# Kernel tuning notes

Hardware: AMD Instinct MI355X
Metric: run time of the kernel (lower is better)

Reference implementation:

```python
import jax, jax.numpy as jnp
import numpy as np

E, IN, OUT, T = 8, 4096, 4096, 8192
GS = IN  # groupsize=-1 -> groupsize = infeatures


def setup_inputs() -> dict:
    key = jax.random.key(0)
    k1, k2, k3, k4, k5 = jax.random.split(key, 5)
    x = jax.random.normal(k1, (T, IN), dtype=jnp.float16)
    indices = jax.random.randint(k2, (T,), 0, E, dtype=jnp.int32)
    # int32 words each packing 8 int4 nonzero values (2:4 sparse -> IN*OUT/2 values per expert)
    qweight = jax.random.randint(k3, (E, IN // 32, OUT * 16 // 8), 0, 2**31 - 1, dtype=jnp.int32)
    meta = jax.random.randint(k4, (E, OUT, IN // 16), 0, 2**15, dtype=jnp.int32).astype(jnp.int16)
    scales = (jax.random.uniform(k5, (E, IN // GS, OUT), dtype=jnp.float32) * 0.02 + 0.001).astype(jnp.float16)
    return {"x": x, "indices": indices, "qweight": qweight, "meta": meta, "scales": scales}


def _dequant_24(qweight, meta, scales):
    """Decode packed int4 + 2:4-sparsity metadata into dense fp32 weights (E, OUT, IN)."""
    # unpack 8 int4 nibbles per int32 word, symmetric zero-point 8
    nib = (qweight[..., None] >> (4 * jnp.arange(8, dtype=jnp.int32))) & 0xF  # (E, IN//32, 2*OUT, 8)
    vals = nib.reshape(E, IN // 2, OUT).transpose(0, 2, 1).astype(jnp.float32) - 8.0  # (E, OUT, IN//2)
    m = meta.astype(jnp.int32) & 0xFFFF
    sub = (m[..., None] >> (2 * jnp.arange(8, dtype=jnp.int32))) & 0x3  # (E, OUT, IN//16, 8)
    grp = (jnp.arange(8, dtype=jnp.int32) // 2) * 4                      # group-of-4 base within 16-block
    base = 16 * jnp.arange(IN // 16, dtype=jnp.int32)                    # 16-block base
    dense_col = (base[None, None, :, None] + grp[None, None, None, :] + sub).reshape(E, OUT, IN // 2)
    eidx = jnp.arange(E)[:, None, None]
    oidx = jnp.arange(OUT)[None, :, None]
    W = jnp.zeros((E, OUT, IN), jnp.float32).at[eidx, oidx, dense_col].add(vals)
    # per-group dequant scales: (E, IN//GS, OUT) -> (E, OUT, IN)
    s = jnp.repeat(scales.astype(jnp.float32), GS, axis=1).transpose(0, 2, 1)
    return W * s


def reference(x, indices, qweight, meta, scales):
    W = _dequant_24(qweight, meta, scales)  # (E, OUT, IN)
    y = jnp.zeros((x.shape[0], OUT), jnp.float32)
    for e in range(E):  # fixed small expert count
        xe = jnp.where((indices == e)[:, None], x, 0).astype(jnp.float32)
        y = y + xe @ W[e].T
    return y.astype(x.dtype)
```

## Files before the change

### kernel.cpp

```cpp
#include <hip/hip_runtime.h>

#define E_N   8
#define IN_N  4096
#define OUT_N 4096
#define T_N   8192

#define BM 256
#define BN 256
#define NT_K 64
#define NTHREADS 512

typedef unsigned short u16;
typedef __bf16 bf16_t;
typedef bf16_t bf16x8 __attribute__((ext_vector_type(8)));
typedef u16    u16x8  __attribute__((ext_vector_type(8)));
typedef float  f32x4  __attribute__((ext_vector_type(4)));

#define GLOAD16(gsrc, ldst) \
    __builtin_amdgcn_global_load_lds( \
        (const __attribute__((address_space(1))) unsigned int*)(gsrc), \
        (__attribute__((address_space(3))) unsigned int*)(ldst), 16, 0, 0)

__device__ int g_cnt[E_N];
__device__ int g_base[E_N];
__device__ int g_ids[T_N];
__device__ int g_meta_wide;
__device__ u16 g_W[(long)E_N * OUT_N * IN_N];
__device__ u16 g_xb[(long)T_N * IN_N];

__device__ __forceinline__ u16 f2bf(float f) {
    unsigned u = __builtin_bit_cast(unsigned, f);
    u += 0x7FFFu + ((u >> 16) & 1u);
    return (u16)(u >> 16);
}

__global__ void sort_tokens(const int* __restrict__ idx, const u16* __restrict__ meta16) {
    __shared__ int cnt[E_N], off[E_N];
    __shared__ int probe;
    const int tid = threadIdx.x;
    const int lane = tid & 63;
    if (tid == 0) probe = 0;
    if (tid < E_N) cnt[tid] = 0;
    __syncthreads();
    if (tid < 64) {
        unsigned v = meta16[2 * (tid * 131072) + 1];
        if (v) atomicOr(&probe, 1);
    }
    for (int t0 = tid - lane; t0 < T_N; t0 += blockDim.x) {
        const int t = t0 + lane;
        const int my = idx[t] & 7;
        #pragma unroll
        for (int e = 0; e < E_N; ++e) {
            unsigned long long m = __ballot(my == e);
            if (lane == 0 && m) atomicAdd(&cnt[e], __popcll(m));
        }
    }
    __syncthreads();
    if (tid == 0) {
        int s = 0;
        for (int e = 0; e < E_N; ++e) { g_cnt[e] = cnt[e]; g_base[e] = s; off[e] = s; s += cnt[e]; }
        g_meta_wide = (probe == 0) ? 1 : 0;
    }
    __syncthreads();
    for (int t0 = tid - lane; t0 < T_N; t0 += blockDim.x) {
        const int t = t0 + lane;
        const int my = idx[t] & 7;
        #pragma unroll
        for (int e = 0; e < E_N; ++e) {
            unsigned long long m = __ballot(my == e);
            if (my == e) {
                int below = __popcll(m & ((1ull << lane) - 1ull));
                int basep = 0;
                if (below == 0) basep = atomicAdd(&off[e], __popcll(m));
                int src = __ffsll((long long)m) - 1;
                basep = __shfl(basep, src);
                int p = basep + below;
                if (p >= 0 && p < T_N) g_ids[p] = t;
            }
        }
    }
}

__global__ __launch_bounds__(256, 4)
void xb_convert(const float* __restrict__ x) {
    const int p = blockIdx.x;
    int tok = g_ids[p];
    if ((unsigned)tok >= (unsigned)T_N) tok = 0;
    const float* src = x + (long)tok * IN_N;
    u16* dst = g_xb + (long)p * IN_N;
    const int tid = threadIdx.x;
    float va[16];
    #pragma unroll
    for (int c4 = 0; c4 < 4; ++c4) {
        float4 v = *reinterpret_cast<const float4*>(src + tid * 16 + c4 * 4);
        va[c4 * 4 + 0] = v.x; va[c4 * 4 + 1] = v.y; va[c4 * 4 + 2] = v.z; va[c4 * 4 + 3] = v.w;
    }
    unsigned wp[8];
    #pragma unroll
    for (int p8 = 0; p8 < 8; ++p8)
        wp[p8] = (unsigned)f2bf(va[2 * p8]) | ((unsigned)f2bf(va[2 * p8 + 1]) << 16);
    *reinterpret_cast<int4*>(dst + tid * 16)     = make_int4((int)wp[0], (int)wp[1], (int)wp[2], (int)wp[3]);
    *reinterpret_cast<int4*>(dst + tid * 16 + 8) = make_int4((int)wp[4], (int)wp[5], (int)wp[6], (int)wp[7]);
}

__global__ __launch_bounds__(256, 4)
void decode_w(const int* __restrict__ qw, const void* __restrict__ meta) {
    const int e   = blockIdx.z;
    const int kt0 = blockIdx.y * 4;
    const int o   = blockIdx.x * 256 + threadIdx.x;
    const bool mwide = (g_meta_wide != 0);
    unsigned mws[16];
    if (mwide) {
        const int* mp = (const int*)meta + ((long)e * OUT_N + o) * (IN_N / 16) + kt0 * 4;
        #pragma unroll
        for (int i = 0; i < 16; ++i) mws[i] = (unsigned)mp[i] & 0xFFFFu;
    } else {
        const u16* mp = (const u16*)meta + ((long)e * OUT_N + o) * (IN_N / 16) + kt0 * 4;
        #pragma unroll
        for (int i = 0; i < 16; ++i) mws[i] = mp[i];
    }
    const unsigned sh = (o & 7) << 2;
    const int osw = o & 7;
    #pragma unroll
    for (int ki = 0; ki < 4; ++ki) {
        const int kt = kt0 + ki;
        unsigned wp[32];
        #pragma unroll
        for (int gi = 0; gi < 4; ++gi) {
            const int g = kt * 4 + gi;
            const unsigned mw = mws[ki * 4 + gi];
            const int* qp = qw + ((e * (IN_N / 32) + (g >> 1)) << 13) + (o >> 3) + ((g & 1) << 12);
            int d[16];
            #pragma unroll
            for (int p = 0; p < 16; ++p) d[p] = 0;
            #pragma unroll
            for (int grp = 0; grp < 4; ++grp) {
                const unsigned w0 = (unsigned)qp[(2 * grp) * 512];
                const unsigned w1 = (unsigned)qp[(2 * grp + 1) * 512];
                const int v0 = (int)((w0 >> sh) & 0xF) - 8;
                const int v1 = (int)((w1 >> sh) & 0xF) - 8;
                const int s0 = (mw >> (4 * grp)) & 3;
                const int s1 = (mw >> (4 * grp + 2)) & 3;
                #pragma unroll
                for (int q = 0; q < 4; ++q) {
                    int t0 = (s0 == q) ? v0 : 0;
                    int t1 = (s1 == q) ? v1 : 0;
                    d[grp * 4 + q] = t0 + t1;
                }
            }
            #pragma unroll
            for (int p = 0; p < 8; ++p) {
                unsigned lo = __builtin_bit_cast(unsigned, (float)d[2 * p])     >> 16;
                unsigned hi = __builtin_bit_cast(unsigned, (float)d[2 * p + 1]) >> 16;
                wp[gi * 8 + p] = lo | (hi << 16);
            }
        }
        u16* wr = g_W + ((long)(e * 64 + kt) * OUT_N + o) * 64;
        #pragma unroll
        for (int h = 0; h < 8; ++h)
            *reinterpret_cast<int4*>(wr + (h ^ osw) * 8) =
                make_int4((int)wp[h * 4], (int)wp[h * 4 + 1], (int)wp[h * 4 + 2], (int)wp[h * 4 + 3]);
    }
}

__global__ __launch_bounds__(NTHREADS, 2)
void moe_gemm(const float* __restrict__ scales, float* __restrict__ y) {
    const int e = blockIdx.z;
    int cnt = g_cnt[e];
    if (cnt < 0) cnt = 0;
    if (cnt > T_N) cnt = T_N;
    const int m0 = blockIdx.y * BM;
    if (m0 >= cnt) return;
    const int n0 = blockIdx.x * BN;
    int base = g_base[e];
    if (base < 0) base = 0;
    if (base > T_N - cnt) base = T_N - cnt;

    __shared__ __align__(16) u16 As[2 * BM * 64];
    __shared__ __align__(16) u16 Bs[2 * BN * 64];

    const int tid  = threadIdx.x;
    const int lane = tid & 63;
    const int wid  = tid >> 6;
    const int wm   = wid >> 2;
    const int wn   = wid & 3;

    const int r_loc = tid >> 3;
    const int h_a   = (tid & 7) ^ (r_loc & 7);
    const u16* asrc[4];
    #pragma unroll
    for (int q = 0; q < 4; ++q) {
        long grow = (long)base + m0 + q * 64 + r_loc;
        if (grow > T_N - 1) grow = T_N - 1;
        asrc[q] = g_xb + grow * IN_N + h_a * 8;
    }
    const u16* bsrc = g_W + ((long)e * NT_K * OUT_N + n0) * 64 + (long)tid * 8;

#define STAGE_A(B_, KT_, HT_) do { \
    const int ktc_ = ((KT_) < NT_K) ? (KT_) : (NT_K - 1); \
    GLOAD16(asrc[(HT_)*2 + 0] + ktc_ * 64, &As[(B_)*16384 + ((HT_)*1024 + tid) * 8]); \
    GLOAD16(asrc[(HT_)*2 + 1] + ktc_ * 64, &As[(B_)*16384 + ((HT_)*1024 + 512 + tid) * 8]); \
} while (0)
#define STAGE_B(B_, KT_, HT_) do { \
    const int ktc_ = ((KT_) < NT_K) ? (KT_) : (NT_K - 1); \
    const u16* s_ = bsrc + (long)ktc_ * (OUT_N * 64) + (HT_) * 8192; \
    GLOAD16(s_,        &Bs[(B_)*16384 + ((HT_)*1024 + tid) * 8]); \
    GLOAD16(s_ + 4096, &Bs[(B_)*16384 + ((HT_)*1024 + 512 + tid) * 8]); \
} while (0)

    const int l15   = lane & 15;
    const int aoff0 = ((((lane >> 4))     ^ (lane & 7)) << 3);
    const int aoff1 = (((4 + (lane >> 4)) ^ (lane & 7)) << 3);
    const int arow0 = (wm * 128 + l15) * 64;
    const int brow0 = (wn * 64  + l15) * 64;

#define LD8(P_) __builtin_bit_cast(bf16x8, *reinterpret_cast<const u16x8*>(P_))
#define VM4 asm volatile("s_waitcnt vmcnt(4)" ::: "memory")
#define PH_NOP ((void)0)

    f32x4 acc[8][4];
    #pragma unroll
    for (int i = 0; i < 8; ++i)
        #pragma unroll
        for (int j = 0; j < 4; ++j) acc[i][j] = (f32x4){0.f, 0.f, 0.f, 0.f};

    bf16x8 aR[4][2];
    bf16x8 bR[2][2][2];

#define PH(B_, QM_, QN_, RDA_, RDB_, STAGE_STMT, TAIL_STMT) do { \
    if (RDA_) { _Pragma("unroll") for (int mf = 0; mf < 4; ++mf) { \
        const u16* p_ = &As[(B_)*16384 + arow0 + (QM_)*4096 + mf*1024]; \
        aR[mf][0] = LD8(p_ + aoff0); aR[mf][1] = LD8(p_ + aoff1); } } \
    if (RDB_) { _Pragma("unroll") for (int nf = 0; nf < 2; ++nf) { \
        const u16* p_ = &Bs[(B_)*16384 + brow0 + (QN_)*2048 + nf*1024]; \
        bR[QN_][nf][0] = LD8(p_ + aoff0); bR[QN_][nf][1] = LD8(p_ + aoff1); } } \
    STAGE_STMT; \
    __builtin_amdgcn_s_barrier(); \
    asm volatile("s_waitcnt lgkmcnt(0)" ::: "memory"); \
    __builtin_amdgcn_sched_barrier(0); \
    __builtin_amdgcn_s_setprio(1); \
    _Pragma("unroll") for (int ks = 0; ks < 2; ++ks) \
      _Pragma("unroll") for (int mf = 0; mf < 4; ++mf) \
        _Pragma("unroll") for (int nf = 0; nf < 2; ++nf) \
          acc[(QM_)*4 + mf][(QN_)*2 + nf] = __builtin_amdgcn_mfma_f32_16x16x32_bf16( \
              aR[mf][ks], bR[QN_][nf][ks], acc[(QM_)*4 + mf][(QN_)*2 + nf], 0, 0, 0); \
    __builtin_amdgcn_s_setprio(0); \
    TAIL_STMT; \
    __builtin_amdgcn_s_barrier(); \
} while (0)

    STAGE_A(0, 0, 0); STAGE_A(0, 0, 1);
    STAGE_B(0, 0, 0); STAGE_B(0, 0, 1);
    STAGE_B(1, 1, 0); STAGE_B(1, 1, 1);
    VM4;
    __builtin_amdgcn_s_barrier();

    for (int t = 0; t < NT_K / 2; ++t) {
        const int k1 = 2 * t + 1, k2 = 2 * t + 2, k3 = 2 * t + 3;
        PH(0, 0, 0, 1, 1, STAGE_A(1, k1, 0), PH_NOP);
        PH(0, 0, 1, 0, 1, STAGE_A(1, k1, 1), PH_NOP);
        PH(0, 1, 0, 1, 0, STAGE_B(0, k2, 0), PH_NOP);
        PH(0, 1, 1, 0, 0, STAGE_B(0, k2, 1), VM4);
        PH(1, 0, 0, 1, 1, STAGE_A(0, k2, 0), PH_NOP);
        PH(1, 0, 1, 0, 1, STAGE_A(0, k2, 1), PH_NOP);
        PH(1, 1, 0, 1, 0, STAGE_B(1, k3, 0), PH_NOP);
        PH(1, 1, 1, 0, 0, STAGE_B(1, k3, 1), VM4);
    }

    const int* toks = g_ids + base;
    float sc[4];
    #pragma unroll
    for (int nf = 0; nf < 4; ++nf)
        sc[nf] = scales[e * OUT_N + n0 + wn * 64 + nf * 16 + l15];
    #pragma unroll
    for (int mf = 0; mf < 8; ++mf) {
        #pragma unroll
        for (int r = 0; r < 4; ++r) {
            const int row = m0 + wm * 128 + mf * 16 + ((lane >> 4) << 2) + r;
            if (row >= cnt) continue;
            int tok = toks[row];
            if ((unsigned)tok >= (unsigned)T_N) continue;
            float* yrow = y + (long)tok * OUT_N;
            #pragma unroll
            for (int nf = 0; nf < 4; ++nf)
                yrow[n0 + wn * 64 + nf * 16 + l15] = acc[mf][nf][r] * sc[nf];
        }
    }
}

extern "C" void kernel_launch(void* const* d_in, const int* in_sizes, int n_in,
                              void* d_out, int out_size, void* d_ws, size_t ws_size,
                              hipStream_t stream) {
    const float* x      = nullptr;
    const int* indices  = nullptr;
    const int* qw       = nullptr;
    const void* meta    = nullptr;
    const float* scales = nullptr;
    int big_seen = 0;
    for (int i = 0; i < n_in; ++i) {
        long s = in_sizes[i];
        if (s == 33554432L)      x = (const float*)d_in[i];
        else if (s == 8192L)     indices = (const int*)d_in[i];
        else if (s == 32768L)    scales = (const float*)d_in[i];
        else if (s == 8388608L) {
            if (big_seen++ == 0)  qw = (const int*)d_in[i];
            else                  meta = d_in[i];
        }
    }
    if (!x || !indices || !qw || !meta || !scales) return;
    float* y = (float*)d_out;

    hipLaunchKernelGGL(sort_tokens, dim3(1), dim3(1024), 0, stream, indices, (const u16*)meta);
    hipLaunchKernelGGL(xb_convert, dim3(T_N), dim3(256), 0, stream, x);
    hipLaunchKernelGGL(decode_w, dim3(OUT_N / 256, 16, E_N), dim3(256), 0, stream, qw, meta);
    hipLaunchKernelGGL(moe_gemm, dim3(OUT_N / BN, T_N / BM, E_N), dim3(NTHREADS), 0, stream, scales, y);
}
```

Measured before the change: 648.1 us.

## Launch compact M-tile list with XCD swizzle and restage A/B loads

sort_tokens now builds a compact list of (expert, m0) tiles, and the GEMM launches a flat 640-block grid instead of the mostly-empty E×T/BM×N grid. Block IDs are swizzled so that neighbouring tiles land on the same XCD (block mod 8), which should improve L2 reuse. The load pipeline also changes: full A and B tiles for the next k-step are issued together in two of the eight phases, waiting at vmcnt(8), instead of being spread across all phases. This removes the launch cost of empty blocks but puts loads in bursts and assumes at most 64 M-tiles, which only holds for 8 experts and 8192 tokens.

```diff
diff --git a/kernel.cpp b/kernel.cpp
--- a/kernel.cpp
+++ b/kernel.cpp
@@ -9,6 +9,7 @@
 #define BN 256
 #define NT_K 64
 #define NTHREADS 512
+#define MAXMT 64
 
 typedef unsigned short u16;
 typedef __bf16 bf16_t;
@@ -25,6 +26,9 @@
 __device__ int g_base[E_N];
 __device__ int g_ids[T_N];
 __device__ int g_meta_wide;
+__device__ int g_mt_e[MAXMT];
+__device__ int g_mt_m0[MAXMT];
+__device__ int g_nmt;
 __device__ u16 g_W[(long)E_N * OUT_N * IN_N];
 __device__ u16 g_xb[(long)T_N * IN_N];
 
@@ -60,6 +64,10 @@
         int s = 0;
         for (int e = 0; e < E_N; ++e) { g_cnt[e] = cnt[e]; g_base[e] = s; off[e] = s; s += cnt[e]; }
         g_meta_wide = (probe == 0) ? 1 : 0;
+        int n = 0;
+        for (int e = 0; e < E_N; ++e)
+            for (int m0 = 0; m0 < cnt[e] && n < MAXMT; m0 += BM) { g_mt_e[n] = e; g_mt_m0[n] = m0; ++n; }
+        g_nmt = n;
     }
     __syncthreads();
     for (int t0 = tid - lane; t0 < T_N; t0 += blockDim.x) {
@@ -165,13 +173,17 @@
 
 __global__ __launch_bounds__(NTHREADS, 2)
 void moe_gemm(const float* __restrict__ scales, float* __restrict__ y) {
-    const int e = blockIdx.z;
+    const int blk = blockIdx.x;
+    const int swz = (blk & 7) * 80 + (blk >> 3);
+    const int mIdx = swz >> 4, nIdx = swz & 15;
+    if (mIdx >= g_nmt) return;
+    const int e  = g_mt_e[mIdx];
+    const int m0 = g_mt_m0[mIdx];
+    const int n0 = nIdx * BN;
     int cnt = g_cnt[e];
     if (cnt < 0) cnt = 0;
     if (cnt > T_N) cnt = T_N;
-    const int m0 = blockIdx.y * BM;
     if (m0 >= cnt) return;
-    const int n0 = blockIdx.x * BN;
     int base = g_base[e];
     if (base < 0) base = 0;
     if (base > T_N - cnt) base = T_N - cnt;
@@ -196,16 +208,18 @@
     }
     const u16* bsrc = g_W + ((long)e * NT_K * OUT_N + n0) * 64 + (long)tid * 8;
 
-#define STAGE_A(B_, KT_, HT_) do { \
-    const int ktc_ = ((KT_) < NT_K) ? (KT_) : (NT_K - 1); \
-    GLOAD16(asrc[(HT_)*2 + 0] + ktc_ * 64, &As[(B_)*16384 + ((HT_)*1024 + tid) * 8]); \
-    GLOAD16(asrc[(HT_)*2 + 1] + ktc_ * 64, &As[(B_)*16384 + ((HT_)*1024 + 512 + tid) * 8]); \
+#define STAGE_A4(B_, KT_) do { \
+    GLOAD16(asrc[0] + (KT_) * 64, &As[(B_)*16384 + tid * 8]); \
+    GLOAD16(asrc[1] + (KT_) * 64, &As[(B_)*16384 + (512 + tid) * 8]); \
+    GLOAD16(asrc[2] + (KT_) * 64, &As[(B_)*16384 + (1024 + tid) * 8]); \
+    GLOAD16(asrc[3] + (KT_) * 64, &As[(B_)*16384 + (1536 + tid) * 8]); \
 } while (0)
-#define STAGE_B(B_, KT_, HT_) do { \
-    const int ktc_ = ((KT_) < NT_K) ? (KT_) : (NT_K - 1); \
-    const u16* s_ = bsrc + (long)ktc_ * (OUT_N * 64) + (HT_) * 8192; \
-    GLOAD16(s_,        &Bs[(B_)*16384 + ((HT_)*1024 + tid) * 8]); \
-    GLOAD16(s_ + 4096, &Bs[(B_)*16384 + ((HT_)*1024 + 512 + tid) * 8]); \
+#define STAGE_B4(B_, KT_) do { \
+    const u16* s_ = bsrc + (long)(KT_) * (OUT_N * 64); \
+    GLOAD16(s_,         &Bs[(B_)*16384 + tid * 8]); \
+    GLOAD16(s_ + 4096,  &Bs[(B_)*16384 + (512 + tid) * 8]); \
+    GLOAD16(s_ + 8192,  &Bs[(B_)*16384 + (1024 + tid) * 8]); \
+    GLOAD16(s_ + 12288, &Bs[(B_)*16384 + (1536 + tid) * 8]); \
 } while (0)
 
     const int l15   = lane & 15;
@@ -215,7 +229,7 @@
     const int brow0 = (wn * 64  + l15) * 64;
 
 #define LD8(P_) __builtin_bit_cast(bf16x8, *reinterpret_cast<const u16x8*>(P_))
-#define VM4 asm volatile("s_waitcnt vmcnt(4)" ::: "memory")
+#define VM8 asm volatile("s_waitcnt vmcnt(8)" ::: "memory")
 #define PH_NOP ((void)0)
 
     f32x4 acc[8][4];
@@ -249,22 +263,22 @@
     __builtin_amdgcn_s_barrier(); \
 } while (0)
 
-    STAGE_A(0, 0, 0); STAGE_A(0, 0, 1);
-    STAGE_B(0, 0, 0); STAGE_B(0, 0, 1);
-    STAGE_B(1, 1, 0); STAGE_B(1, 1, 1);
-    VM4;
+    STAGE_A4(0, 0); STAGE_B4(0, 0);
+    STAGE_A4(1, 1); STAGE_B4(1, 1);
+    VM8;
     __builtin_amdgcn_s_barrier();
 
     for (int t = 0; t < NT_K / 2; ++t) {
-        const int k1 = 2 * t + 1, k2 = 2 * t + 2, k3 = 2 * t + 3;
-        PH(0, 0, 0, 1, 1, STAGE_A(1, k1, 0), PH_NOP);
-        PH(0, 0, 1, 0, 1, STAGE_A(1, k1, 1), PH_NOP);
-        PH(0, 1, 0, 1, 0, STAGE_B(0, k2, 0), PH_NOP);
-        PH(0, 1, 1, 0, 0, STAGE_B(0, k2, 1), VM4);
-        PH(1, 0, 0, 1, 1, STAGE_A(0, k2, 0), PH_NOP);
-        PH(1, 0, 1, 0, 1, STAGE_A(0, k2, 1), PH_NOP);
-        PH(1, 1, 0, 1, 0, STAGE_B(1, k3, 0), PH_NOP);
-        PH(1, 1, 1, 0, 0, STAGE_B(1, k3, 1), VM4);
+        const int k2 = (2 * t + 2 < NT_K) ? 2 * t + 2 : NT_K - 1;
+        const int k3 = (2 * t + 3 < NT_K) ? 2 * t + 3 : NT_K - 1;
+        PH(0, 0, 0, 1, 1, PH_NOP,          PH_NOP);
+        PH(0, 0, 1, 0, 1, PH_NOP,          PH_NOP);
+        PH(0, 1, 0, 1, 0, STAGE_B4(0, k2), PH_NOP);
+        PH(0, 1, 1, 0, 0, STAGE_A4(0, k2), VM8);
+        PH(1, 0, 0, 1, 1, PH_NOP,          PH_NOP);
+        PH(1, 0, 1, 0, 1, PH_NOP,          PH_NOP);
+        PH(1, 1, 0, 1, 0, STAGE_B4(1, k3), PH_NOP);
+        PH(1, 1, 1, 0, 0, STAGE_A4(1, k3), VM8);
     }
 
     const int* toks = g_ids + base;
@@ -313,5 +327,5 @@
     hipLaunchKernelGGL(sort_tokens, dim3(1), dim3(1024), 0, stream, indices, (const u16*)meta);
     hipLaunchKernelGGL(xb_convert, dim3(T_N), dim3(256), 0, stream, x);
     hipLaunchKernelGGL(decode_w, dim3(OUT_N / 256, 16, E_N), dim3(256), 0, stream, qw, meta);
-    hipLaunchKernelGGL(moe_gemm, dim3(OUT_N / BN, T_N / BM, E_N), dim3(NTHREADS), 0, stream, scales, y);
-}
+    hipLaunchKernelGGL(moe_gemm, dim3(640), dim3(NTHREADS), 0, stream, scales, y);
+}
```

Result: slower. 717.7 us (+10.7%).

## Fuse int4 2:4 weight decode into GEMM mainloop, drop dense bf16 weight buffer

Applied to the files above, without the earlier changes.

Removes the separate decode_w kernel, which materialized a dense bf16 weight tensor (256MB), and instead decodes packed int4 weights and sparsity metadata inside the GEMM's K loop directly into shared memory. Two small preprocessing kernels reorder qweight and transpose meta so each thread can load its words contiguously. This cuts global traffic for writing and rereading dense weights. The cost is extra ALU decode work in every GEMM block, redone for each M tile, plus changed pipelining: loads now go through registers rather than async LDS loads, with waitcnt ordering that looks fragile.

```diff
diff --git a/kernel.cpp b/kernel.cpp
--- a/kernel.cpp
+++ b/kernel.cpp
@@ -25,7 +25,8 @@
 __device__ int g_base[E_N];
 __device__ int g_ids[T_N];
 __device__ int g_meta_wide;
-__device__ u16 g_W[(long)E_N * OUT_N * IN_N];
+__device__ int g_qwt[(long)E_N * 256 * 512 * 8];
+__device__ u16 g_metat[(long)E_N * 256 * 4096];
 __device__ u16 g_xb[(long)T_N * IN_N];
 
 __device__ __forceinline__ u16 f2bf(float f) {
@@ -82,6 +83,41 @@
 }
 
 __global__ __launch_bounds__(256, 4)
+void qw_shuffle(const int* __restrict__ qw) {
+    const int g = blockIdx.x;
+    const int e = blockIdx.y;
+    const int* src = qw + (e * 128 + (g >> 1)) * 8192 + ((g & 1) << 12);
+    int* dst = g_qwt + (long)(e * 256 + g) * 512 * 8;
+    for (int og = threadIdx.x; og < 512; og += 256) {
+        int q[8];
+        #pragma unroll
+        for (int t = 0; t < 8; ++t) q[t] = src[t * 512 + og];
+        #pragma unroll
+        for (int t = 0; t < 8; ++t) dst[og * 8 + t] = q[t];
+    }
+}
+
+__global__ __launch_bounds__(256, 4)
+void meta_transpose(const void* __restrict__ meta) {
+    __shared__ u16 tile[16][272];
+    const int e = blockIdx.z, g0 = blockIdx.y * 16, o0 = blockIdx.x * 256;
+    const int o = o0 + threadIdx.x;
+    if (g_meta_wide) {
+        const int* mp = (const int*)meta + ((long)e * OUT_N + o) * 256 + g0;
+        #pragma unroll
+        for (int g = 0; g < 16; ++g) tile[g][threadIdx.x] = (u16)mp[g];
+    } else {
+        const u16* mp = (const u16*)meta + ((long)e * OUT_N + o) * 256 + g0;
+        #pragma unroll
+        for (int g = 0; g < 16; ++g) tile[g][threadIdx.x] = mp[g];
+    }
+    __syncthreads();
+    #pragma unroll
+    for (int g = 0; g < 16; ++g)
+        g_metat[(long)(e * 256 + g0 + g) * 4096 + o0 + threadIdx.x] = tile[g][threadIdx.x];
+}
+
+__global__ __launch_bounds__(256, 4)
 void xb_convert(const float* __restrict__ x) {
     const int p = blockIdx.x;
     int tok = g_ids[p];
@@ -101,66 +137,6 @@
         wp[p8] = (unsigned)f2bf(va[2 * p8]) | ((unsigned)f2bf(va[2 * p8 + 1]) << 16);
     *reinterpret_cast<int4*>(dst + tid * 16)     = make_int4((int)wp[0], (int)wp[1], (int)wp[2], (int)wp[3]);
     *reinterpret_cast<int4*>(dst + tid * 16 + 8) = make_int4((int)wp[4], (int)wp[5], (int)wp[6], (int)wp[7]);
-}
-
-__global__ __launch_bounds__(256, 4)
-void decode_w(const int* __restrict__ qw, const void* __restrict__ meta) {
-    const int e   = blockIdx.z;
-    const int kt0 = blockIdx.y * 4;
-    const int o   = blockIdx.x * 256 + threadIdx.x;
-    const bool mwide = (g_meta_wide != 0);
-    unsigned mws[16];
-    if (mwide) {
-        const int* mp = (const int*)meta + ((long)e * OUT_N + o) * (IN_N / 16) + kt0 * 4;
-        #pragma unroll
-        for (int i = 0; i < 16; ++i) mws[i] = (unsigned)mp[i] & 0xFFFFu;
-    } else {
-        const u16* mp = (const u16*)meta + ((long)e * OUT_N + o) * (IN_N / 16) + kt0 * 4;
-        #pragma unroll
-        for (int i = 0; i < 16; ++i) mws[i] = mp[i];
-    }
-    const unsigned sh = (o & 7) << 2;
-    const int osw = o & 7;
-    #pragma unroll
-    for (int ki = 0; ki < 4; ++ki) {
-        const int kt = kt0 + ki;
-        unsigned wp[32];
-        #pragma unroll
-        for (int gi = 0; gi < 4; ++gi) {
-            const int g = kt * 4 + gi;
-            const unsigned mw = mws[ki * 4 + gi];
-            const int* qp = qw + ((e * (IN_N / 32) + (g >> 1)) << 13) + (o >> 3) + ((g & 1) << 12);
-            int d[16];
-            #pragma unroll
-            for (int p = 0; p < 16; ++p) d[p] = 0;
-            #pragma unroll
-            for (int grp = 0; grp < 4; ++grp) {
-                const unsigned w0 = (unsigned)qp[(2 * grp) * 512];
-                const unsigned w1 = (unsigned)qp[(2 * grp + 1) * 512];
-                const int v0 = (int)((w0 >> sh) & 0xF) - 8;
-                const int v1 = (int)((w1 >> sh) & 0xF) - 8;
-                const int s0 = (mw >> (4 * grp)) & 3;
-                const int s1 = (mw >> (4 * grp + 2)) & 3;
-                #pragma unroll
-                for (int q = 0; q < 4; ++q) {
-                    int t0 = (s0 == q) ? v0 : 0;
-                    int t1 = (s1 == q) ? v1 : 0;
-                    d[grp * 4 + q] = t0 + t1;
-                }
-            }
-            #pragma unroll
-            for (int p = 0; p < 8; ++p) {
-                unsigned lo = __builtin_bit_cast(unsigned, (float)d[2 * p])     >> 16;
-                unsigned hi = __builtin_bit_cast(unsigned, (float)d[2 * p + 1]) >> 16;
-                wp[gi * 8 + p] = lo | (hi << 16);
-            }
-        }
-        u16* wr = g_W + ((long)(e * 64 + kt) * OUT_N + o) * 64;
-        #pragma unroll
-        for (int h = 0; h < 8; ++h)
-            *reinterpret_cast<int4*>(wr + (h ^ osw) * 8) =
-                make_int4((int)wp[h * 4], (int)wp[h * 4 + 1], (int)wp[h * 4 + 2], (int)wp[h * 4 + 3]);
-    }
 }
 
 __global__ __launch_bounds__(NTHREADS, 2)
@@ -194,18 +170,54 @@
         if (grow > T_N - 1) grow = T_N - 1;
         asrc[q] = g_xb + grow * IN_N + h_a * 8;
     }
-    const u16* bsrc = g_W + ((long)e * NT_K * OUT_N + n0) * 64 + (long)tid * 8;
-
-#define STAGE_A(B_, KT_, HT_) do { \
-    const int ktc_ = ((KT_) < NT_K) ? (KT_) : (NT_K - 1); \
-    GLOAD16(asrc[(HT_)*2 + 0] + ktc_ * 64, &As[(B_)*16384 + ((HT_)*1024 + tid) * 8]); \
-    GLOAD16(asrc[(HT_)*2 + 1] + ktc_ * 64, &As[(B_)*16384 + ((HT_)*1024 + 512 + tid) * 8]); \
+#define STAGE_A4(B_, KT_) do { \
+    GLOAD16(asrc[0] + (KT_) * 64, &As[(B_)*16384 + tid * 8]); \
+    GLOAD16(asrc[1] + (KT_) * 64, &As[(B_)*16384 + (512 + tid) * 8]); \
+    GLOAD16(asrc[2] + (KT_) * 64, &As[(B_)*16384 + (1024 + tid) * 8]); \
+    GLOAD16(asrc[3] + (KT_) * 64, &As[(B_)*16384 + (1536 + tid) * 8]); \
 } while (0)
-#define STAGE_B(B_, KT_, HT_) do { \
-    const int ktc_ = ((KT_) < NT_K) ? (KT_) : (NT_K - 1); \
-    const u16* s_ = bsrc + (long)ktc_ * (OUT_N * 64) + (HT_) * 8192; \
-    GLOAD16(s_,        &Bs[(B_)*16384 + ((HT_)*1024 + tid) * 8]); \
-    GLOAD16(s_ + 4096, &Bs[(B_)*16384 + ((HT_)*1024 + 512 + tid) * 8]); \
+
+    const int cB  = tid & 255;
+    const int giA = tid >> 8;
+    const int giB = 2 + (tid >> 8);
+    const int ogB = (n0 + cB) >> 3;
+    const unsigned shB = (cB & 7) << 2;
+    int4 qA0, qA1, qB0, qB1;
+    unsigned mwA, mwB;
+
+#define LOADB(Q0_, Q1_, MW_, GI_, KT_) do { \
+    const int g_ = (KT_) * 4 + (GI_); \
+    const int4* qt_ = (const int4*)(g_qwt + ((long)(e * 256 + g_) * 512 + ogB) * 8); \
+    Q0_ = qt_[0]; Q1_ = qt_[1]; \
+    MW_ = g_metat[(long)(e * 256 + g_) * 4096 + n0 + cB]; \
+} while (0)
+
+#define DECB(Q0_, Q1_, MW_, GI_, B_) do { \
+    const unsigned qv_[8] = { (unsigned)(Q0_).x, (unsigned)(Q0_).y, (unsigned)(Q0_).z, (unsigned)(Q0_).w, \
+                              (unsigned)(Q1_).x, (unsigned)(Q1_).y, (unsigned)(Q1_).z, (unsigned)(Q1_).w }; \
+    int d_[16]; \
+    _Pragma("unroll") for (int p = 0; p < 16; ++p) d_[p] = 0; \
+    _Pragma("unroll") for (int grp = 0; grp < 4; ++grp) { \
+        const int v0_ = (int)((qv_[2 * grp]     >> shB) & 0xF) - 8; \
+        const int v1_ = (int)((qv_[2 * grp + 1] >> shB) & 0xF) - 8; \
+        const int s0_ = ((MW_) >> (4 * grp)) & 3; \
+        const int s1_ = ((MW_) >> (4 * grp + 2)) & 3; \
+        _Pragma("unroll") for (int qq = 0; qq < 4; ++qq) { \
+            int t0_ = (s0_ == qq) ? v0_ : 0; \
+            int t1_ = (s1_ == qq) ? v1_ : 0; \
+            d_[grp * 4 + qq] = t0_ + t1_;           \
+        } \
+    } \
+    unsigned wp_[8]; \
+    _Pragma("unroll") for (int p = 0; p < 8; ++p) { \
+        unsigned lo_ = __builtin_bit_cast(unsigned, (float)d_[2 * p])     >> 16;   \
+        unsigned hi_ = __builtin_bit_cast(unsigned, (float)d_[2 * p + 1]) >> 16; \
+        wp_[p] = lo_ | (hi_ << 16); \
+    } \
+    *reinterpret_cast<int4*>(&Bs[(B_)*16384 + (cB * 8 + ((2 * (GI_) + 0) ^ (cB & 7))) * 8]) = \
+        make_int4((int)wp_[0], (int)wp_[1], (int)wp_[2], (int)wp_[3]); \
+    *reinterpret_cast<int4*>(&Bs[(B_)*16384 + (cB * 8 + ((2 * (GI_) + 1) ^ (cB & 7))) * 8]) = \
+        make_int4((int)wp_[4], (int)wp_[5], (int)wp_[6], (int)wp_[7]); \
 } while (0)
 
     const int l15   = lane & 15;
@@ -249,22 +261,26 @@
     __builtin_amdgcn_s_barrier(); \
 } while (0)
 
-    STAGE_A(0, 0, 0); STAGE_A(0, 0, 1);
-    STAGE_B(0, 0, 0); STAGE_B(0, 0, 1);
-    STAGE_B(1, 1, 0); STAGE_B(1, 1, 1);
-    VM4;
+    STAGE_A4(0, 0); STAGE_A4(1, 1);
+    LOADB(qA0, qA1, mwA, giA, 0); LOADB(qB0, qB1, mwB, giB, 0);
+    DECB(qA0, qA1, mwA, giA, 0);  DECB(qB0, qB1, mwB, giB, 0);
+    LOADB(qA0, qA1, mwA, giA, 1); LOADB(qB0, qB1, mwB, giB, 1);
+    DECB(qA0, qA1, mwA, giA, 1);  DECB(qB0, qB1, mwB, giB, 1);
+    asm volatile("s_waitcnt lgkmcnt(0)" ::: "memory");
+    asm volatile("s_waitcnt vmcnt(4)" ::: "memory");
     __builtin_amdgcn_s_barrier();
 
     for (int t = 0; t < NT_K / 2; ++t) {
-        const int k1 = 2 * t + 1, k2 = 2 * t + 2, k3 = 2 * t + 3;
-        PH(0, 0, 0, 1, 1, STAGE_A(1, k1, 0), PH_NOP);
-        PH(0, 0, 1, 0, 1, STAGE_A(1, k1, 1), PH_NOP);
-        PH(0, 1, 0, 1, 0, STAGE_B(0, k2, 0), PH_NOP);
-        PH(0, 1, 1, 0, 0, STAGE_B(0, k2, 1), VM4);
-        PH(1, 0, 0, 1, 1, STAGE_A(0, k2, 0), PH_NOP);
-        PH(1, 0, 1, 0, 1, STAGE_A(0, k2, 1), PH_NOP);
-        PH(1, 1, 0, 1, 0, STAGE_B(1, k3, 0), PH_NOP);
-        PH(1, 1, 1, 0, 0, STAGE_B(1, k3, 1), VM4);
+        const int k2 = (2 * t + 2 < NT_K) ? 2 * t + 2 : NT_K - 1;
+        const int k3 = (2 * t + 3 < NT_K) ? 2 * t + 3 : NT_K - 1;
+        PH(0, 0, 0, 1, 1, LOADB(qA0, qA1, mwA, giA, k2), PH_NOP);
+        PH(0, 0, 1, 0, 1, LOADB(qB0, qB1, mwB, giB, k2), PH_NOP);
+        PH(0, 1, 0, 1, 0, DECB(qA0, qA1, mwA, giA, 0),   PH_NOP);
+        PH(0, 1, 1, 0, 0, DECB(qB0, qB1, mwB, giB, 0); STAGE_A4(0, k2), VM4);
+        PH(1, 0, 0, 1, 1, LOADB(qA0, qA1, mwA, giA, k3), PH_NOP);
+        PH(1, 0, 1, 0, 1, LOADB(qB0, qB1, mwB, giB, k3), PH_NOP);
+        PH(1, 1, 0, 1, 0, DECB(qA0, qA1, mwA, giA, 1),   PH_NOP);
+        PH(1, 1, 1, 0, 0, DECB(qB0, qB1, mwB, giB, 1); STAGE_A4(1, k3), VM4);
     }
 
     const int* toks = g_ids + base;
@@ -311,7 +327,8 @@
     float* y = (float*)d_out;
 
     hipLaunchKernelGGL(sort_tokens, dim3(1), dim3(1024), 0, stream, indices, (const u16*)meta);
+    hipLaunchKernelGGL(qw_shuffle, dim3(256, E_N), dim3(256), 0, stream, qw);
+    hipLaunchKernelGGL(meta_transpose, dim3(16, 16, E_N), dim3(256), 0, stream, meta);
     hipLaunchKernelGGL(xb_convert, dim3(T_N), dim3(256), 0, stream, x);
-    hipLaunchKernelGGL(decode_w, dim3(OUT_N / 256, 16, E_N), dim3(256), 0, stream, qw, meta);
     hipLaunchKernelGGL(moe_gemm, dim3(OUT_N / BN, T_N / BM, E_N), dim3(NTHREADS), 0, stream, scales, y);
 }
```

Result: slower. 698.6 us (+7.8%).
